# Optimization experiments

Measured on AMD Instinct MI355X. Metric: run time of the kernel, lower is better.

## Reference

```python
import jax, jax.numpy as jnp
import numpy as np

N, C, T, V = 16, 64, 512, 25
R, O, S = 8, 64, 3  # rel_channels, out_channels, num_subset


def setup_inputs() -> dict:
    key = jax.random.key(0)
    ks = jax.random.split(key, 12)
    sc = 0.05
    return {
        "x": jax.random.normal(ks[0], (N, C, T, V), jnp.float32),
        "A": jax.random.normal(ks[1], (S, V, V), jnp.float32) * 0.1,
        "alpha": jax.random.normal(ks[2], (1,), jnp.float32) * 0.1,
        "w1": jax.random.normal(ks[3], (S, R, C), jnp.float32) * sc,
        "b1": jax.random.normal(ks[4], (S, R), jnp.float32) * sc,
        "w2": jax.random.normal(ks[5], (S, R, C), jnp.float32) * sc,
        "b2": jax.random.normal(ks[6], (S, R), jnp.float32) * sc,
        "w3": jax.random.normal(ks[7], (S, O, C), jnp.float32) * sc,
        "b3": jax.random.normal(ks[8], (S, O), jnp.float32) * sc,
        "w4": jax.random.normal(ks[9], (S, O, R), jnp.float32) * sc,
        "b4": jax.random.normal(ks[10], (S, O), jnp.float32) * sc,
        "sparse": 0,
    }


def _mask(w, thr):
    # SparseConv2d: magnitude-threshold the 1x1 conv weights at runtime.
    return jnp.where(jnp.abs(w) > thr, w, jnp.zeros_like(w))


def reference(x, A, alpha, w1, b1, w2, b2, w3, b3, w4, b4, sparse):
    thr = jnp.float32(sparse)

    def conv1x1(w, b, inp):  # w [o,c], b [o], inp [n,c,t,v] -> [n,o,t,v]
        return jnp.einsum('oc,nctv->notv', _mask(w, thr), inp) + b[None, :, None, None]

    y = None
    for i in range(A.shape[0]):
        x1 = conv1x1(w1[i], b1[i], x).mean(-2)          # [n,r,v]
        x2 = conv1x1(w2[i], b2[i], x).mean(-2)          # [n,r,v]
        x3 = conv1x1(w3[i], b3[i], x)                   # [n,o,t,v]
        att = jnp.tanh(x1[..., :, None] - x2[..., None, :])  # [n,r,v,v]
        a = jnp.einsum('or,nruv->nouv', _mask(w4[i], thr), att) + b4[i][None, :, None, None]
        a = a * alpha + A[i][None, None]                # [n,o,v,v]
        z = jnp.einsum('ncuv,nctu->nctv', a, x3)        # node aggregation
        y = z if y is None else y + z
    # in_channels == out_channels -> residual is identity
    return jax.nn.relu(y + x)
```

## Files before the change

kernel.cpp:

```cpp
#include <hip/hip_runtime.h>
#include <cmath>

typedef __bf16 bf16x8 __attribute__((ext_vector_type(8)));
typedef float f32x4 __attribute__((ext_vector_type(4)));

namespace {
constexpr int kN = 16, kC = 64, kT = 512, kV = 25, kS = 3, kR = 8, kO = 64;
constexpr int kTV = kT * kV;
constexpr int kTT = 16;
constexpr size_t WS_AFRAG = 102400;
constexpr size_t WS_W3F = WS_AFRAG + (size_t)48 * 131072;
}

__device__ __forceinline__ int swzA(int col, int cbyte) {
  return ((col << 7) + cbyte) ^ ((col & 7) << 4);
}
__device__ __forceinline__ int swzB(int c, int t, int ubyte) {
  return 65536 + (c << 10) + (((t << 6) + ubyte) ^ ((t & 7) << 4));
}

__global__ __launch_bounds__(512) void k1_mean(const float* __restrict__ x,
                                               float* __restrict__ xm) {
  const int bid = blockIdx.x;
  __shared__ float tile[kTV];
  __shared__ float part[25][20];
  const int tid = threadIdx.x;
  const float4* xg4 = (const float4*)(x + (size_t)bid * kTV);
  for (int i4 = tid; i4 < 3200; i4 += 512) ((float4*)tile)[i4] = xg4[i4];
  __syncthreads();
  if (tid < 500) {
    const int v = tid / 20, k = tid % 20;
    float psum = 0.f;
    for (int t = k; t < kT; t += 20) psum += tile[t * 25 + v];
    part[v][k] = psum;
  }
  __syncthreads();
  if (tid < 25) {
    float s = 0.f;
#pragma unroll
    for (int kk = 0; kk < 20; ++kk) s += part[tid][kk];
    xm[bid * 25 + tid] = s * (1.f / 512.f);
  }
}

__global__ __launch_bounds__(256) void k2_attn(
    const float* __restrict__ xm, const float* __restrict__ Ag,
    const float* __restrict__ alpha, const float* __restrict__ w1,
    const float* __restrict__ b1, const float* __restrict__ w2,
    const float* __restrict__ b2, const float* __restrict__ w3,
    const float* __restrict__ w4, const float* __restrict__ b4,
    const int* __restrict__ sparse, unsigned char* __restrict__ ws) {
  const float thr = (float)sparse[0];
  const int b = blockIdx.x;
  const int s = b >> 6, n = (b >> 2) & 15, q = b & 3;
  __shared__ float xm_l[1600];
  __shared__ float x1_l[200], x2_l[200];
  __shared__ float att_l[8 * 625];
  __shared__ float attsum_l[200];
  __shared__ float ag_l[625];
  __shared__ float acs_l[25];
  __shared__ float w4_l[512];
  const int tid = threadIdx.x;
  for (int i = tid; i < 1600; i += 256) xm_l[i] = xm[n * 1600 + i];
  for (int i = tid; i < 512; i += 256) {
    float w = w4[s * 512 + i];
    w4_l[i] = (fabsf(w) > thr) ? w : 0.f;
  }
  for (int i = tid; i < 625; i += 256) ag_l[i] = Ag[s * 625 + i];
  __syncthreads();
  for (int i = tid; i < 400; i += 256) {
    int which = i / 200, idx = i % 200, r = idx / 25, u = idx % 25;
    const float* wrow = (which == 0 ? w1 : w2) + (s * 8 + r) * 64;
    float acc = 0.f;
    for (int cc = 0; cc < 64; ++cc) {
      float w = wrow[cc];
      w = (fabsf(w) > thr) ? w : 0.f;
      acc += w * xm_l[cc * 25 + u];
    }
    acc += (which == 0 ? b1 : b2)[s * 8 + r];
    if (which == 0) x1_l[idx] = acc;
    else x2_l[idx] = acc;
  }
  __syncthreads();
  for (int i = tid; i < 8 * 625; i += 256) {
    int r = i / 625, uv = i % 625, u = uv / 25, v = uv % 25;
    att_l[i] = tanhf(x1_l[r * 25 + u] - x2_l[r * 25 + v]);
  }
  __syncthreads();
  if (tid < 200) {
    int r = tid / 25, v = tid % 25;
    float sum = 0.f;
    for (int u = 0; u < 25; ++u) sum += att_l[r * 625 + u * 25 + v];
    attsum_l[tid] = sum;
  } else if (tid < 225) {
    int v = tid - 200;
    float sum = 0.f;
    for (int u = 0; u < 25; ++u) sum += ag_l[u * 25 + v];
    acs_l[v] = sum;
  }
  __syncthreads();
  const float al = alpha[0];
  unsigned char* afrag = ws + WS_AFRAG + (size_t)(s * 16 + n) * 131072;
  for (int slot = q * 2048 + tid; slot < (q + 1) * 2048; slot += 256) {
    int c = slot >> 7, vt = (slot >> 6) & 1, l = slot & 63;
    int v = vt * 16 + (l & 15), g = l >> 4;
    bf16x8 out;
    if (v < 25) {
      float b4v = b4[s * 64 + c];
#pragma unroll
      for (int j = 0; j < 8; ++j) {
        int u = g * 8 + j;
        float val = 0.f;
        if (u < 25) {
          float acc = 0.f;
#pragma unroll
          for (int r = 0; r < 8; ++r) acc += w4_l[c * 8 + r] * att_l[r * 625 + u * 25 + v];
          val = al * (acc + b4v) + ag_l[u * 25 + v];
        } else if (u == 25) {
          float acc = 0.f;
#pragma unroll
          for (int r = 0; r < 8; ++r) acc += w4_l[c * 8 + r] * attsum_l[r * 25 + v];
          val = al * acc + 25.f * al * b4v + acs_l[v];
        }
        out[j] = (__bf16)val;
      }
    } else {
#pragma unroll
      for (int j = 0; j < 8; ++j) out[j] = (__bf16)0.f;
    }
    *(bf16x8*)(afrag + (size_t)slot * 16) = out;
  }
  if (n == 0 && tid < 128) {
    unsigned char* w3f = ws + WS_W3F + (size_t)s * 8192;
    int slot = q * 128 + tid;
    int ot = slot >> 7, ks = (slot >> 6) & 1, l = slot & 63;
    int o = ot * 16 + (l & 15), g = l >> 4;
    bf16x8 out;
#pragma unroll
    for (int j = 0; j < 8; ++j) {
      int cp = ks * 32 + g * 8 + j;
      float w = w3[(s * 64 + o) * 64 + cp];
      out[j] = (__bf16)((fabsf(w) > thr) ? w : 0.f);
    }
    *(bf16x8*)(w3f + slot * 16) = out;
  }
}

__global__ __launch_bounds__(512, 2) void k3_main(const float* __restrict__ x,
                                                  const float* __restrict__ b3,
                                                  const unsigned char* __restrict__ ws,
                                                  float* __restrict__ y) {
  const int n = blockIdx.x;
  const int tb = blockIdx.y;
  extern __shared__ __align__(16) unsigned char smem[];
  const int tid = threadIdx.x;
  const int w = tid >> 6, l = tid & 63, g = l >> 4, l15 = l & 15;

  const float4* xg4 = (const float4*)(x + (size_t)n * kC * kTV);

  for (int idx = tid; idx < 3072; idx += 512) {
    int c = idx / 48, r = idx % 48, t = r / 3, ub = 52 + (r % 3) * 4;
    *(unsigned int*)(smem + swzB(c, t, ub)) = 0u;
  }
  for (int i4 = tid; i4 < 6400; i4 += 512) {
    int c = i4 / 100, r4 = i4 % 100;
    float4 vv = xg4[c * 3200 + tb * 100 + r4];
    float vals[4] = {vv.x, vv.y, vv.z, vv.w};
    int lin = r4 * 4;
#pragma unroll
    for (int kk = 0; kk < 4; ++kk) {
      int t = (lin + kk) / 25, u = (lin + kk) % 25;
      *(__bf16*)(smem + swzA(t * 32 + u, c * 2)) = (__bf16)vals[kk];
    }
  }
  __syncthreads();

  const unsigned char* afrag = ws + WS_AFRAG;
  const unsigned char* w3f = ws + WS_W3F;

  f32x4 zacc[8][2];
#pragma unroll
  for (int cc = 0; cc < 8; ++cc)
#pragma unroll
    for (int vt = 0; vt < 2; ++vt) {
      f32x4 zz = {0.f, 0.f, 0.f, 0.f};
      zacc[cc][vt] = zz;
    }

  for (int s = 0; s < kS; ++s) {
    bf16x8 A1[4][2];
#pragma unroll
    for (int ot = 0; ot < 4; ++ot)
#pragma unroll
      for (int ks = 0; ks < 2; ++ks)
        A1[ot][ks] = *(const bf16x8*)(w3f + s * 8192 + ((ot * 2 + ks) * 64 + l) * 16);
    if (s) __syncthreads();

    f32x4 acc[4][4];
#pragma unroll
    for (int cti = 0; cti < 4; ++cti) {
      int col = w * 64 + cti * 16 + l15;
      bf16x8 bk0 = *(const bf16x8*)(smem + swzA(col, g * 16));
      bf16x8 bk1 = *(const bf16x8*)(smem + swzA(col, 64 + g * 16));
#pragma unroll
      for (int ot = 0; ot < 4; ++ot) {
        f32x4 d = {0.f, 0.f, 0.f, 0.f};
        d = __builtin_amdgcn_mfma_f32_16x16x32_bf16(A1[ot][0], bk0, d, 0, 0, 0);
        d = __builtin_amdgcn_mfma_f32_16x16x32_bf16(A1[ot][1], bk1, d, 0, 0, 0);
        acc[cti][ot] = d;
      }
    }
#pragma unroll
    for (int cti = 0; cti < 4; ++cti) {
      int col = w * 64 + cti * 16 + l15;
      int t = col >> 5, u = col & 31;
      if (u < 25) {
#pragma unroll
        for (int ot = 0; ot < 4; ++ot)
#pragma unroll
          for (int jj = 0; jj < 4; ++jj) {
            int o = ot * 16 + g * 4 + jj;
            *(__bf16*)(smem + swzB(o, t, u * 2)) = (__bf16)acc[cti][ot][jj];
          }
      }
    }
    for (int slot = tid; slot < 1024; slot += 512) {
      int c = slot >> 4, t = slot & 15;
      *(__bf16*)(smem + swzB(c, t, 50)) = (__bf16)b3[s * 64 + c];
    }
    bf16x8 B2[8][2];
    const unsigned char* af = afrag + (size_t)(s * 16 + n) * 131072;
#pragma unroll
    for (int cc = 0; cc < 8; ++cc) {
      int c = w * 8 + cc;
#pragma unroll
      for (int vt = 0; vt < 2; ++vt)
        B2[cc][vt] = *(const bf16x8*)(af + ((c * 2 + vt) * 64 + l) * 16);
    }
    __syncthreads();
#pragma unroll
    for (int cc = 0; cc < 8; ++cc) {
      int c = w * 8 + cc;
      bf16x8 a2 = *(const bf16x8*)(smem + swzB(c, l15, g * 16));
      zacc[cc][0] = __builtin_amdgcn_mfma_f32_16x16x32_bf16(a2, B2[cc][0], zacc[cc][0], 0, 0, 0);
      zacc[cc][1] = __builtin_amdgcn_mfma_f32_16x16x32_bf16(a2, B2[cc][1], zacc[cc][1], 0, 0, 0);
    }
  }
  __syncthreads();
  float* zs = (float*)smem;
#pragma unroll
  for (int cc = 0; cc < 8; ++cc) {
    int c = w * 8 + cc;
#pragma unroll
    for (int vt = 0; vt < 2; ++vt) {
      int v = vt * 16 + l15;
      if (v < 25) {
#pragma unroll
        for (int jj = 0; jj < 4; ++jj) {
          int t = g * 4 + jj;
          zs[c * 400 + t * 25 + v] = zacc[cc][vt][jj];
        }
      }
    }
  }
  __syncthreads();
  float4* yg4 = (float4*)(y + (size_t)n * kC * kTV);
  for (int i4 = tid; i4 < 6400; i4 += 512) {
    int c = i4 / 100, r4 = i4 % 100;
    float4 xv = xg4[c * 3200 + tb * 100 + r4];
    float4 zv = *(const float4*)(zs + c * 400 + r4 * 4);
    float4 o;
    o.x = fmaxf(zv.x + xv.x, 0.f);
    o.y = fmaxf(zv.y + xv.y, 0.f);
    o.z = fmaxf(zv.z + xv.z, 0.f);
    o.w = fmaxf(zv.w + xv.w, 0.f);
    yg4[c * 3200 + tb * 100 + r4] = o;
  }
}

extern "C" void kernel_launch(void* const* d_in, const int* in_sizes, int n_in,
                              void* d_out, int out_size, void* d_ws, size_t ws_size,
                              hipStream_t stream) {
  const float* x = (const float*)d_in[0];
  const float* Ag = (const float*)d_in[1];
  const float* alpha = (const float*)d_in[2];
  const float* w1 = (const float*)d_in[3];
  const float* b1 = (const float*)d_in[4];
  const float* w2 = (const float*)d_in[5];
  const float* b2 = (const float*)d_in[6];
  const float* w3 = (const float*)d_in[7];
  const float* b3 = (const float*)d_in[8];
  const float* w4 = (const float*)d_in[9];
  const float* b4 = (const float*)d_in[10];
  const int* sparse = (const int*)d_in[11];

  unsigned char* ws = (unsigned char*)d_ws;
  float* xm = (float*)ws;
  float* y = (float*)d_out;

  static bool attr_set = false;
  if (!attr_set) {
    hipFuncSetAttribute((const void*)k3_main,
                        hipFuncAttributeMaxDynamicSharedMemorySize, 131072);
    attr_set = true;
  }

  k1_mean<<<kN * kC, 512, 0, stream>>>(x, xm);
  k2_attn<<<kS * kN * 4, 256, 0, stream>>>(xm, Ag, alpha, w1, b1, w2, b2, w3, w4,
                                           b4, sparse, ws);
  dim3 g3(kN, kT / kTT);
  k3_main<<<g3, 512, 131072, stream>>>(x, b3, ws, y);
}
```

Baseline: 88.27 us.

## Rework mean reduction, swizzle, conv-output packing and fused residual epilogue

k1_mean now reduces straight from global memory with per-thread float4 accumulators instead of staging the whole tile in LDS. In k3_main the swizzle of the second LDS buffer now mixes in the channel index, and the MFMA operands are swapped so each lane writes conv outputs as packed bf16x4 rather than scalar bf16. The padding columns of the x tile are zeroed explicitly. The epilogue drops the fp32 LDS round-trip and the global re-read of x, adding the residual from the bf16 copy of x already held in LDS and writing y directly. This trades coalesced float4 stores for strided scalar stores and uses a bf16-rounded residual, which may cost accuracy.

```diff
diff --git a/kernel.cpp b/kernel.cpp
--- a/kernel.cpp
+++ b/kernel.cpp
@@ -1,13 +1,13 @@
 #include <hip/hip_runtime.h>
 #include <cmath>
 
+typedef __bf16 bf16x4v __attribute__((ext_vector_type(4)));
 typedef __bf16 bf16x8 __attribute__((ext_vector_type(8)));
 typedef float f32x4 __attribute__((ext_vector_type(4)));
 
 namespace {
-constexpr int kN = 16, kC = 64, kT = 512, kV = 25, kS = 3, kR = 8, kO = 64;
+constexpr int kN = 16, kC = 64, kT = 512, kV = 25, kS = 3, kO = 64;
 constexpr int kTV = kT * kV;
-constexpr int kTT = 16;
 constexpr size_t WS_AFRAG = 102400;
 constexpr size_t WS_W3F = WS_AFRAG + (size_t)48 * 131072;
 }
@@ -16,29 +16,32 @@
   return ((col << 7) + cbyte) ^ ((col & 7) << 4);
 }
 __device__ __forceinline__ int swzB(int c, int t, int ubyte) {
-  return 65536 + (c << 10) + (((t << 6) + ubyte) ^ ((t & 7) << 4));
-}
-
-__global__ __launch_bounds__(512) void k1_mean(const float* __restrict__ x,
+  return 65536 + (c << 10) + (((t << 6) + ubyte) ^ ((((c ^ t) & 7)) << 4));
+}
+
+__global__ __launch_bounds__(256) void k1_mean(const float* __restrict__ x,
                                                float* __restrict__ xm) {
   const int bid = blockIdx.x;
-  __shared__ float tile[kTV];
-  __shared__ float part[25][20];
+  __shared__ float part[250][4];
   const int tid = threadIdx.x;
   const float4* xg4 = (const float4*)(x + (size_t)bid * kTV);
-  for (int i4 = tid; i4 < 3200; i4 += 512) ((float4*)tile)[i4] = xg4[i4];
-  __syncthreads();
-  if (tid < 500) {
-    const int v = tid / 20, k = tid % 20;
-    float psum = 0.f;
-    for (int t = k; t < kT; t += 20) psum += tile[t * 25 + v];
-    part[v][k] = psum;
+  if (tid < 250) {
+    float a0 = 0.f, a1 = 0.f, a2 = 0.f, a3 = 0.f;
+    for (int j = tid; j < 3200; j += 250) {
+      float4 v = xg4[j];
+      a0 += v.x; a1 += v.y; a2 += v.z; a3 += v.w;
+    }
+    part[tid][0] = a0; part[tid][1] = a1; part[tid][2] = a2; part[tid][3] = a3;
   }
   __syncthreads();
   if (tid < 25) {
     float s = 0.f;
 #pragma unroll
-    for (int kk = 0; kk < 20; ++kk) s += part[tid][kk];
+    for (int r = 0; r < 4; ++r) {
+      int q = ((tid - r + 25) % 25) * 19 % 25;
+#pragma unroll
+      for (int p = 0; p < 10; ++p) s += part[q + 25 * p][r];
+    }
     xm[bid * 25 + tid] = s * (1.f / 512.f);
   }
 }
@@ -146,21 +149,27 @@
   }
 }
 
-__global__ __launch_bounds__(512, 2) void k3_main(const float* __restrict__ x,
-                                                  const float* __restrict__ b3,
-                                                  const unsigned char* __restrict__ ws,
-                                                  float* __restrict__ y) {
+__global__ __launch_bounds__(512) void k3_main(const float* __restrict__ x,
+                                               const float* __restrict__ b3,
+                                               const unsigned char* __restrict__ ws,
+                                               float* __restrict__ y) {
   const int n = blockIdx.x;
   const int tb = blockIdx.y;
   extern __shared__ __align__(16) unsigned char smem[];
   const int tid = threadIdx.x;
   const int w = tid >> 6, l = tid & 63, g = l >> 4, l15 = l & 15;
-
   const float4* xg4 = (const float4*)(x + (size_t)n * kC * kTV);
 
+  for (int idx = tid; idx < 3584; idx += 512) {
+    int col_i = idx >> 3, gb = idx & 7;
+    int t = col_i / 7, u = 25 + col_i % 7;
+    f32x4 z = {0.f, 0.f, 0.f, 0.f};
+    *(f32x4*)(smem + swzA(t * 32 + u, gb * 16)) = z;
+  }
   for (int idx = tid; idx < 3072; idx += 512) {
-    int c = idx / 48, r = idx % 48, t = r / 3, ub = 52 + (r % 3) * 4;
-    *(unsigned int*)(smem + swzB(c, t, ub)) = 0u;
+    int pair = idx / 3, k = idx % 3;
+    int c = pair >> 4, t = pair & 15;
+    *(unsigned int*)(smem + swzB(c, t, 52 + 4 * k)) = 0u;
   }
   for (int i4 = tid; i4 < 6400; i4 += 512) {
     int c = i4 / 100, r4 = i4 % 100;
@@ -168,9 +177,9 @@
     float vals[4] = {vv.x, vv.y, vv.z, vv.w};
     int lin = r4 * 4;
 #pragma unroll
-    for (int kk = 0; kk < 4; ++kk) {
-      int t = (lin + kk) / 25, u = (lin + kk) % 25;
-      *(__bf16*)(smem + swzA(t * 32 + u, c * 2)) = (__bf16)vals[kk];
+    for (int k = 0; k < 4; ++k) {
+      int t = (lin + k) / 25, u = (lin + k) % 25;
+      *(__bf16*)(smem + swzA(t * 32 + u, c * 2)) = (__bf16)vals[k];
     }
   }
   __syncthreads();
@@ -200,28 +209,33 @@
 #pragma unroll
     for (int cti = 0; cti < 4; ++cti) {
       int col = w * 64 + cti * 16 + l15;
-      bf16x8 bk0 = *(const bf16x8*)(smem + swzA(col, g * 16));
-      bf16x8 bk1 = *(const bf16x8*)(smem + swzA(col, 64 + g * 16));
+      bf16x8 xa0 = *(const bf16x8*)(smem + swzA(col, g * 16));
+      bf16x8 xa1 = *(const bf16x8*)(smem + swzA(col, 64 + g * 16));
 #pragma unroll
       for (int ot = 0; ot < 4; ++ot) {
         f32x4 d = {0.f, 0.f, 0.f, 0.f};
-        d = __builtin_amdgcn_mfma_f32_16x16x32_bf16(A1[ot][0], bk0, d, 0, 0, 0);
-        d = __builtin_amdgcn_mfma_f32_16x16x32_bf16(A1[ot][1], bk1, d, 0, 0, 0);
+        d = __builtin_amdgcn_mfma_f32_16x16x32_bf16(xa0, A1[ot][0], d, 0, 0, 0);
+        d = __builtin_amdgcn_mfma_f32_16x16x32_bf16(xa1, A1[ot][1], d, 0, 0, 0);
         acc[cti][ot] = d;
       }
     }
 #pragma unroll
     for (int cti = 0; cti < 4; ++cti) {
-      int col = w * 64 + cti * 16 + l15;
-      int t = col >> 5, u = col & 31;
-      if (u < 25) {
-#pragma unroll
-        for (int ot = 0; ot < 4; ++ot)
-#pragma unroll
-          for (int jj = 0; jj < 4; ++jj) {
-            int o = ot * 16 + g * 4 + jj;
-            *(__bf16*)(smem + swzB(o, t, u * 2)) = (__bf16)acc[cti][ot][jj];
-          }
+      int t = 2 * w + (cti >> 1);
+      int u0 = (cti & 1) * 16 + g * 4;
+#pragma unroll
+      for (int ot = 0; ot < 4; ++ot) {
+        int c = ot * 16 + l15;
+        if (!(cti & 1) || g < 2) {
+          bf16x4v pk;
+          pk[0] = (__bf16)acc[cti][ot][0];
+          pk[1] = (__bf16)acc[cti][ot][1];
+          pk[2] = (__bf16)acc[cti][ot][2];
+          pk[3] = (__bf16)acc[cti][ot][3];
+          *(bf16x4v*)(smem + swzB(c, t, 2 * u0)) = pk;
+        } else if (g == 2) {
+          *(__bf16*)(smem + swzB(c, t, 48)) = (__bf16)acc[cti][ot][0];
+        }
       }
     }
     for (int slot = tid; slot < 1024; slot += 512) {
@@ -246,35 +260,21 @@
       zacc[cc][1] = __builtin_amdgcn_mfma_f32_16x16x32_bf16(a2, B2[cc][1], zacc[cc][1], 0, 0, 0);
     }
   }
-  __syncthreads();
-  float* zs = (float*)smem;
-#pragma unroll
-  for (int cc = 0; cc < 8; ++cc) {
-    int c = w * 8 + cc;
-#pragma unroll
-    for (int vt = 0; vt < 2; ++vt) {
-      int v = vt * 16 + l15;
+#pragma unroll
+  for (int vt = 0; vt < 2; ++vt) {
+    int v = vt * 16 + l15;
+#pragma unroll
+    for (int jj = 0; jj < 4; ++jj) {
+      int t = g * 4 + jj;
+      bf16x8 xr = *(const bf16x8*)(smem + swzA(t * 32 + v, w * 16));
       if (v < 25) {
 #pragma unroll
-        for (int jj = 0; jj < 4; ++jj) {
-          int t = g * 4 + jj;
-          zs[c * 400 + t * 25 + v] = zacc[cc][vt][jj];
+        for (int cc = 0; cc < 8; ++cc) {
+          float o = fmaxf(zacc[cc][vt][jj] + (float)xr[cc], 0.f);
+          y[((size_t)n * 64 + w * 8 + cc) * kTV + (tb * 16 + t) * 25 + v] = o;
         }
       }
     }
-  }
-  __syncthreads();
-  float4* yg4 = (float4*)(y + (size_t)n * kC * kTV);
-  for (int i4 = tid; i4 < 6400; i4 += 512) {
-    int c = i4 / 100, r4 = i4 % 100;
-    float4 xv = xg4[c * 3200 + tb * 100 + r4];
-    float4 zv = *(const float4*)(zs + c * 400 + r4 * 4);
-    float4 o;
-    o.x = fmaxf(zv.x + xv.x, 0.f);
-    o.y = fmaxf(zv.y + xv.y, 0.f);
-    o.z = fmaxf(zv.z + xv.z, 0.f);
-    o.w = fmaxf(zv.w + xv.w, 0.f);
-    yg4[c * 3200 + tb * 100 + r4] = o;
   }
 }
 
@@ -298,16 +298,12 @@
   float* xm = (float*)ws;
   float* y = (float*)d_out;
 
-  static bool attr_set = false;
-  if (!attr_set) {
-    hipFuncSetAttribute((const void*)k3_main,
-                        hipFuncAttributeMaxDynamicSharedMemorySize, 131072);
-    attr_set = true;
-  }
-
-  k1_mean<<<kN * kC, 512, 0, stream>>>(x, xm);
+  hipFuncSetAttribute((const void*)k3_main,
+                      hipFuncAttributeMaxDynamicSharedMemorySize, 131072);
+
+  k1_mean<<<kN * kC, 256, 0, stream>>>(x, xm);
   k2_attn<<<kS * kN * 4, 256, 0, stream>>>(xm, Ag, alpha, w1, b1, w2, b2, w3, w4,
                                            b4, sparse, ws);
-  dim3 g3(kN, kT / kTT);
+  dim3 g3(kN, kT / 16);
   k3_main<<<g3, 512, 131072, stream>>>(x, b3, ws, y);
 }
```

Measured after the change: 77.93 us. 1.13x faster.
